# Performance work log

Measured on AMD Instinct MI355X. Metric: run time of the kernel, lower is better.

The kernel has to match this reference:

```python
import jax, jax.numpy as jnp
import numpy as np

N_ATOMS = 100000
N_PAIRS = 6400000
NBATCH = 16
RC = 3.0
SIGMA = 1.0
EPSILON = 1.0


def setup_inputs() -> dict:
    key = jax.random.key(0)
    k1, k2, k3 = jax.random.split(key, 3)
    # distances in a physical range (0.8, 3.0), strictly positive, below cutoff rc
    dist = jax.random.uniform(k1, (N_PAIRS,), dtype=jnp.float32, minval=0.8, maxval=RC)
    ind_1 = jax.random.randint(k2, (N_ATOMS, 1), 0, NBATCH, dtype=jnp.int64)
    ind_2 = jax.random.randint(k3, (N_PAIRS, 2), 0, N_ATOMS, dtype=jnp.int64)
    return {"dist": dist, "ind_1": ind_1, "ind_2": ind_2}


def reference(dist, ind_1, ind_2):
    rc, sigma, epsilon = RC, SIGMA, EPSILON
    # energy shift so the potential is zero at the cutoff radius
    e0 = 4.0 * epsilon * ((sigma / rc) ** 12 - (sigma / rc) ** 6)
    c6 = (sigma / dist) ** 6          # [n_pairs]
    c12 = c6 * c6
    en = 4.0 * epsilon * (c12 - c6) - e0
    natom = ind_1.shape[0]            # static
    # scatter per-pair energy onto first atom of each pair
    en_atom = jax.ops.segment_sum(en, ind_2[:, 0], num_segments=natom)
    return en_atom / 2.0
```

## Files before the change

### kernel.cpp

```cpp
#include <hip/hip_runtime.h>


#define CHUNK 8192
#define T1 512
#define ABITS 11
#define APB 2048
#define NBMAX 63
#define QSCALE 32768.0f
#define QINV (1.0f / 32768.0f)
#define S_SLICES 32

static __device__ __forceinline__ float half_en(float d) {
    const float half_e0 = -2.739720872119788e-3f;
    float inv = 1.0f / d;
    float i2 = inv * inv;
    float i6 = i2 * i2 * i2;
    return 2.0f * (i6 * i6 - i6) - half_e0;
}

static __device__ __forceinline__ int quant(float e) {
    int q = __float2int_rn(e * QSCALE);
    return max(-1048576, min(1048575, q));
}

__global__ __launch_bounds__(T1) void lj_bin(const float* __restrict__ dist,
                                             const int* __restrict__ ind2,
                                             unsigned* __restrict__ grec,
                                             unsigned* __restrict__ goffs,
                                             int n_pairs, int nblk, int nb) {
    __shared__ unsigned cnt[NBMAX + 1];
    __shared__ unsigned offs[NBMAX + 1];
    __shared__ unsigned recs[CHUNK];

    const int t = threadIdx.x;
    const int c = blockIdx.x;
    const int base = c * CHUNK;

    if (t <= NBMAX) cnt[t] = 0;
    __syncthreads();

    unsigned rec[16];
    unsigned br[16];

    #pragma unroll
    for (int g = 0; g < 4; ++g) {
        const int p0 = base + g * (T1 * 4) + t * 4;
        float dd[4] = {0.f, 0.f, 0.f, 0.f};
        int ii[4] = {0, 0, 0, 0};
        if (p0 + 4 <= n_pairs) {
            float4 d = *reinterpret_cast<const float4*>(dist + p0);
            int4 ia = *reinterpret_cast<const int4*>(ind2 + 2 * p0);
            int4 ib = *reinterpret_cast<const int4*>(ind2 + 2 * p0 + 4);
            dd[0] = d.x; dd[1] = d.y; dd[2] = d.z; dd[3] = d.w;
            ii[0] = ia.x; ii[1] = ia.z; ii[2] = ib.x; ii[3] = ib.z;
        } else {
            #pragma unroll
            for (int k = 0; k < 4; ++k)
                if (p0 + k < n_pairs) { dd[k] = dist[p0 + k]; ii[k] = ind2[2 * (p0 + k)]; }
        }
        #pragma unroll
        for (int k = 0; k < 4; ++k) {
            const int j = g * 4 + k;
            if (p0 + k < n_pairs) {
                const int id = ii[k];
                const int b = id >> ABITS;
                const int q = quant(half_en(dd[k]));
                rec[j] = (((unsigned)q) << ABITS) | (unsigned)(id & (APB - 1));
                const unsigned rank = atomicAdd(&cnt[b], 1u);
                br[j] = ((unsigned)b << 16) | rank;
            } else {
                br[j] = 0xFFFFFFFFu;
                rec[j] = 0;
            }
        }
    }
    __syncthreads();

    if (t < 64) {
        const unsigned v = cnt[t];
        unsigned inc = v;
        #pragma unroll
        for (int d = 1; d < 64; d <<= 1) {
            const unsigned x = __shfl_up(inc, d, 64);
            if (t >= d) inc += x;
        }
        offs[t] = inc - v;
    }
    __syncthreads();

    #pragma unroll
    for (int j = 0; j < 16; ++j) {
        if (br[j] != 0xFFFFFFFFu) {
            const unsigned pos = offs[br[j] >> 16] + (br[j] & 0xFFFFu);
            recs[pos] = rec[j];
        }
    }
    __syncthreads();

    const int nv = min(CHUNK, n_pairs - base);
    for (int i4 = t * 4; i4 + 4 <= nv; i4 += T1 * 4) {
        uint4 v = *reinterpret_cast<const uint4*>(&recs[i4]);
        *reinterpret_cast<uint4*>(&grec[(size_t)base + i4]) = v;
    }
    for (int i = (nv & ~3) + t; i < nv; i += T1)
        grec[(size_t)base + i] = recs[i];
    if (t <= nb)
        goffs[(size_t)t * nblk + c] = offs[t];
}

__global__ __launch_bounds__(256) void lj_bucket_reduce(const unsigned* __restrict__ grec,
                                                        const unsigned* __restrict__ goffs,
                                                        int* __restrict__ partial,
                                                        int nblk, int nb, int natom_pad,
                                                        int cps) {
    __shared__ int acc[APB];
    const int t = threadIdx.x;
    const int b = blockIdx.x % nb;
    const int s = blockIdx.x / nb;

    #pragma unroll
    for (int k = 0; k < APB / 256; ++k) acc[t + k * 256] = 0;
    __syncthreads();

    const unsigned* r0 = goffs + (size_t)b * nblk;
    const unsigned* r1 = goffs + (size_t)(b + 1) * nblk;
    const int c0 = s * cps;
    const int c1 = min(nblk, c0 + cps);
    const int wv = t >> 6;
    const int ln = t & 63;

    for (int c = c0 + wv; c < c1; c += 4) {
        const unsigned o0 = r0[c];
        const unsigned o1 = r1[c];
        const size_t rb = (size_t)c * CHUNK;
        for (unsigned i = o0 + ln; i < o1; i += 64) {
            const unsigned r = grec[rb + i];
            atomicAdd(&acc[r & (APB - 1)], ((int)r) >> ABITS);
        }
    }
    __syncthreads();

    int* dst = partial + (size_t)s * natom_pad + (size_t)b * APB;
    #pragma unroll
    for (int k = 0; k < APB / 256; ++k) dst[t + k * 256] = acc[t + k * 256];
}

__global__ void lj_final(const int* __restrict__ partial, float* __restrict__ out,
                         int natom, int natom_pad) {
    const int a = blockIdx.x * blockDim.x + threadIdx.x;
    if (a >= natom) return;
    int ssum = 0;
    #pragma unroll
    for (int s = 0; s < S_SLICES; ++s)
        ssum += partial[(size_t)s * natom_pad + a];
    out[a] = (float)ssum * QINV;
}

__global__ void lj_scatter_direct(const float* __restrict__ dist,
                                  const int* __restrict__ ind2,
                                  float* __restrict__ out,
                                  int n_pairs) {
    int t = blockIdx.x * blockDim.x + threadIdx.x;
    int i = t * 4;
    if (i >= n_pairs) return;
    if (i + 4 <= n_pairs) {
        float4 d = *reinterpret_cast<const float4*>(dist + i);
        int4 ia = *reinterpret_cast<const int4*>(ind2 + 2 * i);
        int4 ib = *reinterpret_cast<const int4*>(ind2 + 2 * i + 4);
        atomicAdd(&out[ia.x], half_en(d.x));
        atomicAdd(&out[ia.z], half_en(d.y));
        atomicAdd(&out[ib.x], half_en(d.z));
        atomicAdd(&out[ib.z], half_en(d.w));
    } else {
        for (int p = i; p < n_pairs; ++p)
            atomicAdd(&out[ind2[2 * p]], half_en(dist[p]));
    }
}

extern "C" void kernel_launch(void* const* d_in, const int* in_sizes, int n_in,
                              void* d_out, int out_size, void* d_ws, size_t ws_size,
                              hipStream_t stream) {
    const float* dist = (const float*)d_in[0];
    const int* ind2 = (const int*)d_in[2];
    float* out = (float*)d_out;

    const int n_pairs = in_sizes[0];
    const int natom = out_size;

    const int nblk = (n_pairs + CHUNK - 1) / CHUNK;
    const int nb = (natom + APB - 1) / APB;
    const int natom_pad = nb * APB;
    const int cps = (nblk + S_SLICES - 1) / S_SLICES;

    const size_t rec_bytes = (size_t)nblk * CHUNK * sizeof(unsigned);
    const size_t offs_bytes = (size_t)(nb + 1) * nblk * sizeof(unsigned);
    const size_t part_bytes = (size_t)S_SLICES * natom_pad * sizeof(int);
    const size_t need = rec_bytes + offs_bytes + part_bytes;

    if (nb > NBMAX || need > ws_size) {
        hipMemsetAsync(d_out, 0, (size_t)out_size * sizeof(float), stream);
        int n_threads = (n_pairs + 3) / 4;
        int grid = (n_threads + 255) / 256;
        lj_scatter_direct<<<grid, 256, 0, stream>>>(dist, ind2, out, n_pairs);
        return;
    }

    unsigned* grec = (unsigned*)d_ws;
    unsigned* goffs = (unsigned*)((char*)d_ws + rec_bytes);
    int* partial = (int*)((char*)d_ws + rec_bytes + offs_bytes);

    lj_bin<<<nblk, T1, 0, stream>>>(dist, ind2, grec, goffs, n_pairs, nblk, nb);
    lj_bucket_reduce<<<S_SLICES * nb, 256, 0, stream>>>(grec, goffs, partial,
                                                        nblk, nb, natom_pad, cps);
    int fgrid = (natom + 255) / 256;
    lj_final<<<fgrid, 256, 0, stream>>>(partial, out, natom, natom_pad);
}
```

Baseline: 43.35 us.

## Use finer atom buckets, fewer reduce slices, and stage offsets in LDS

Shrinks atom buckets from 2048 to 512 atoms, so there are about 196 buckets instead of 49. This requires a multi-wave prefix scan over 256 bin counters in the binning kernel, and it frees more quantization bits. The reduce kernel now uses 8 slices instead of 32 and preloads each slice's per-chunk offset ranges into dynamic shared memory before scanning records. The aim is fewer partial arrays to sum in the final pass, smaller per-block accumulators, and fewer global offset loads. In exchange, each block now has more record segments to walk per bucket, and binning may have more LDS atomic contention and an extra barrier.

```diff
diff --git a/kernel.cpp b/kernel.cpp
--- a/kernel.cpp
+++ b/kernel.cpp
@@ -3,12 +3,12 @@
 
 #define CHUNK 8192
 #define T1 512
-#define ABITS 11
-#define APB 2048
-#define NBMAX 63
+#define ABITS 9
+#define APB 512
+#define NBMAX 255
 #define QSCALE 32768.0f
 #define QINV (1.0f / 32768.0f)
-#define S_SLICES 32
+#define S_SLICES 8
 
 static __device__ __forceinline__ float half_en(float d) {
     const float half_e0 = -2.739720872119788e-3f;
@@ -20,7 +20,7 @@
 
 static __device__ __forceinline__ int quant(float e) {
     int q = __float2int_rn(e * QSCALE);
-    return max(-1048576, min(1048575, q));
+    return max(-4194304, min(4194303, q));
 }
 
 __global__ __launch_bounds__(T1) void lj_bin(const float* __restrict__ dist,
@@ -28,15 +28,16 @@
                                              unsigned* __restrict__ grec,
                                              unsigned* __restrict__ goffs,
                                              int n_pairs, int nblk, int nb) {
-    __shared__ unsigned cnt[NBMAX + 1];
-    __shared__ unsigned offs[NBMAX + 1];
+    __shared__ unsigned cnt[256];
+    __shared__ unsigned offs[256];
+    __shared__ unsigned wsum[4];
     __shared__ unsigned recs[CHUNK];
 
     const int t = threadIdx.x;
     const int c = blockIdx.x;
     const int base = c * CHUNK;
 
-    if (t <= NBMAX) cnt[t] = 0;
+    if (t < 256) cnt[t] = 0;
     __syncthreads();
 
     unsigned rec[16];
@@ -76,15 +77,23 @@
     }
     __syncthreads();
 
-    if (t < 64) {
-        const unsigned v = cnt[t];
+    {
+        const unsigned v = (t < 256) ? cnt[t] : 0u;
         unsigned inc = v;
         #pragma unroll
         for (int d = 1; d < 64; d <<= 1) {
             const unsigned x = __shfl_up(inc, d, 64);
-            if (t >= d) inc += x;
-        }
-        offs[t] = inc - v;
+            if ((t & 63) >= d) inc += x;
+        }
+        if (t < 256 && (t & 63) == 63) wsum[t >> 6] = inc;
+        __syncthreads();
+        if (t < 256) {
+            unsigned add = 0;
+            #pragma unroll
+            for (int j = 0; j < 4; ++j)
+                if (j < (t >> 6)) add += wsum[j];
+            offs[t] = add + inc - v;
+        }
     }
     __syncthreads();
 
@@ -108,31 +117,50 @@
         goffs[(size_t)t * nblk + c] = offs[t];
 }
 
-__global__ __launch_bounds__(256) void lj_bucket_reduce(const unsigned* __restrict__ grec,
-                                                        const unsigned* __restrict__ goffs,
-                                                        int* __restrict__ partial,
-                                                        int nblk, int nb, int natom_pad,
-                                                        int cps) {
+#define T2 256
+
+__global__ __launch_bounds__(T2) void lj_bucket_reduce(const unsigned* __restrict__ grec,
+                                                       const unsigned* __restrict__ goffs,
+                                                       int* __restrict__ partial,
+                                                       int nblk, int nb, int natom_pad,
+                                                       int cps) {
     __shared__ int acc[APB];
+    extern __shared__ unsigned dynoffs[];
+
     const int t = threadIdx.x;
     const int b = blockIdx.x % nb;
     const int s = blockIdx.x / nb;
 
     #pragma unroll
-    for (int k = 0; k < APB / 256; ++k) acc[t + k * 256] = 0;
-    __syncthreads();
-
-    const unsigned* r0 = goffs + (size_t)b * nblk;
-    const unsigned* r1 = goffs + (size_t)(b + 1) * nblk;
+    for (int k = 0; k < APB / T2; ++k) acc[t + k * T2] = 0;
+
     const int c0 = s * cps;
-    const int c1 = min(nblk, c0 + cps);
+    const int cn = min(nblk - c0, cps);
+    if (cn <= 0) {
+        __syncthreads();
+        int* dst = partial + (size_t)s * natom_pad + (size_t)b * APB;
+        #pragma unroll
+        for (int k = 0; k < APB / T2; ++k) dst[t + k * T2] = acc[t + k * T2];
+        return;
+    }
+
+    unsigned* lo = dynoffs;
+    unsigned* hi = dynoffs + cps;
+    const unsigned* r0 = goffs + (size_t)b * nblk + c0;
+    const unsigned* r1 = goffs + (size_t)(b + 1) * nblk + c0;
+    for (int i = t; i < cn; i += T2) {
+        lo[i] = r0[i];
+        hi[i] = r1[i];
+    }
+    __syncthreads();
+
     const int wv = t >> 6;
     const int ln = t & 63;
 
-    for (int c = c0 + wv; c < c1; c += 4) {
-        const unsigned o0 = r0[c];
-        const unsigned o1 = r1[c];
-        const size_t rb = (size_t)c * CHUNK;
+    for (int c = wv; c < cn; c += T2 / 64) {
+        const unsigned o0 = lo[c];
+        const unsigned o1 = hi[c];
+        const size_t rb = (size_t)(c0 + c) * CHUNK;
         for (unsigned i = o0 + ln; i < o1; i += 64) {
             const unsigned r = grec[rb + i];
             atomicAdd(&acc[r & (APB - 1)], ((int)r) >> ABITS);
@@ -142,7 +170,7 @@
 
     int* dst = partial + (size_t)s * natom_pad + (size_t)b * APB;
     #pragma unroll
-    for (int k = 0; k < APB / 256; ++k) dst[t + k * 256] = acc[t + k * 256];
+    for (int k = 0; k < APB / T2; ++k) dst[t + k * T2] = acc[t + k * T2];
 }
 
 __global__ void lj_final(const int* __restrict__ partial, float* __restrict__ out,
@@ -196,8 +224,9 @@
     const size_t offs_bytes = (size_t)(nb + 1) * nblk * sizeof(unsigned);
     const size_t part_bytes = (size_t)S_SLICES * natom_pad * sizeof(int);
     const size_t need = rec_bytes + offs_bytes + part_bytes;
-
-    if (nb > NBMAX || need > ws_size) {
+    const size_t dyn_lds = 2u * (size_t)cps * sizeof(unsigned);
+
+    if (nb + 1 > 256 || need > ws_size || dyn_lds > 64 * 1024) {
         hipMemsetAsync(d_out, 0, (size_t)out_size * sizeof(float), stream);
         int n_threads = (n_pairs + 3) / 4;
         int grid = (n_threads + 255) / 256;
@@ -210,8 +239,8 @@
     int* partial = (int*)((char*)d_ws + rec_bytes + offs_bytes);
 
     lj_bin<<<nblk, T1, 0, stream>>>(dist, ind2, grec, goffs, n_pairs, nblk, nb);
-    lj_bucket_reduce<<<S_SLICES * nb, 256, 0, stream>>>(grec, goffs, partial,
-                                                        nblk, nb, natom_pad, cps);
+    lj_bucket_reduce<<<S_SLICES * nb, T2, dyn_lds, stream>>>(grec, goffs, partial,
+                                                             nblk, nb, natom_pad, cps);
     int fgrid = (natom + 255) / 256;
     lj_final<<<fgrid, 256, 0, stream>>>(partial, out, natom, natom_pad);
 }
```

Result: no change. 43.21 us (-0.3%).
